# Kernel optimization log

Measured on AMD Instinct MI355X. Metric: run time of the kernel, lower is better.

The kernel has to match this reference:

```python
import jax, jax.numpy as jnp
import numpy as np

N, E = 40000, 640000
S_IN, V_IN = 64, 32            # input irreps: 64x0e + 32x1o (dim 160)
S_MID, V_MID = 96, 128         # tp output: (64+32)x0e, (64+32+32)x1o
S_OUT, V_OUT = 96, 32          # gate irreps_in: 64x0e scalars + 32x0e gates + 32x1o gated
R = 64                         # edge scalar (radial basis) dim
FC_HID = 64
W_NUMEL = 64 + 64 + 32 + 32 + 32  # per-edge tp weights ('uvu', v=1): 224
NUM_NEIGHBORS = 16.0


def setup_inputs() -> dict:
    key = jax.random.key(0)
    ks = jax.random.split(key, 13)
    return {
        "node_features": jax.random.normal(ks[0], (N, S_IN + 3 * V_IN), jnp.float32),
        "node_attr": jnp.ones((N, 1), jnp.float32),
        "edge_src": jax.random.randint(ks[1], (E,), 0, N),
        "edge_dst": jax.random.randint(ks[2], (E,), 0, N),
        "edge_attr": jax.random.normal(ks[3], (E, 4), jnp.float32),
        "edge_scalars": jax.random.normal(ks[4], (E, R), jnp.float32),
        "lin1_ws": jax.random.normal(ks[5], (S_IN, S_IN), jnp.float32),
        "lin1_wv": jax.random.normal(ks[6], (V_IN, V_IN), jnp.float32),
        "fc_w1": jax.random.normal(ks[7], (R, FC_HID), jnp.float32),
        "fc_w2": jax.random.normal(ks[8], (FC_HID, W_NUMEL), jnp.float32),
        "sc_ws": jax.random.normal(ks[9], (S_IN, S_OUT), jnp.float32),
        "sc_wv": jax.random.normal(ks[10], (V_IN, V_OUT), jnp.float32),
        "lin2_ws": jax.random.normal(ks[11], (S_MID, S_OUT), jnp.float32),
        "lin2_wv": jax.random.normal(ks[12], (V_MID, V_OUT), jnp.float32),
    }


def _inv(d):
    return 1.0 / jnp.sqrt(jnp.float32(d))


def _forward(node_features, node_attr, edge_attr, edge_scalars,
             lin1_ws, lin1_wv, fc_w1, fc_w2, sc_ws, sc_wv, lin2_ws, lin2_wv,
             edge_src, edge_dst):
    n = node_features.shape[0]
    s = node_features[:, :S_IN]                      # [N,64] 0e
    v = node_features[:, S_IN:].reshape(n, V_IN, 3)  # [N,32,3] 1o
    a = node_attr                                    # [N,1] scalar node attr

    # self-connection: FullyConnectedTensorProduct(input, 1x0e attr, out) == per-irrep linear
    sc_s = (s @ sc_ws) * a * _inv(S_IN)                                    # [N,96]
    sc_v = jnp.einsum('nci,cd->ndi', v, sc_wv) * a[:, :, None] * _inv(V_IN)  # [N,32,3]

    # lin1
    h_s = (s @ lin1_ws) * a * _inv(S_IN)
    h_v = jnp.einsum('nci,cd->ndi', v, lin1_wv) * a[:, :, None] * _inv(V_IN)

    # per-edge tensor-product weights from FC on edge scalars (silu MLP, no bias)
    hid = jax.nn.silu((edge_scalars @ fc_w1) * _inv(R))
    w = (hid @ fc_w2) * _inv(FC_HID)                 # [E,224]
    w1, w2, w3, w4, w5 = jnp.split(w, [64, 128, 160, 192], axis=-1)

    # gather source node features
    es = h_s[edge_src]                               # [E,64]
    ev = h_v[edge_src]                               # [E,32,3]
    e0 = edge_attr[:, :1]                            # [E,1]  0e
    e1 = edge_attr[:, 1:4]                           # [E,3]  1o

    # Clebsch-Gordan tensor product paths ('uvu', per-edge weights)
    m_s1 = w1 * es * e0                                                   # 0e x 0e -> 0e [E,64]
    m_s2 = w4 * jnp.einsum('eci,ei->ec', ev, e1) * _inv(3)                # 1o x 1o -> 0e [E,32]
    m_v1 = (w2 * es)[:, :, None] * e1[:, None, :]                         # 0e x 1o -> 1o [E,64,3]
    m_v2 = w3[:, :, None] * ev * e0[:, :, None]                           # 1o x 0e -> 1o [E,32,3]
    m_v3 = w5[:, :, None] * jnp.cross(ev, e1[:, None, :]) * _inv(2)       # 1o x 1o -> 1o [E,32,3]

    mid_s = jnp.concatenate([m_s1, m_s2], axis=-1)        # [E,96]
    mid_v = jnp.concatenate([m_v1, m_v2, m_v3], axis=1)   # [E,128,3]

    # scatter-sum to destination nodes, normalized by sqrt(num_neighbors)
    inv_nn = 1.0 / jnp.sqrt(jnp.float32(NUM_NEIGHBORS))
    agg_s = jax.ops.segment_sum(mid_s, edge_dst, num_segments=n) * inv_nn
    agg_v = jax.ops.segment_sum(mid_v, edge_dst, num_segments=n) * inv_nn

    # lin2
    o_s = (agg_s @ lin2_ws) * a * _inv(S_MID)                                  # [N,96]
    o_v = jnp.einsum('nci,cd->ndi', agg_v, lin2_wv) * a[:, :, None] * _inv(V_MID)  # [N,32,3]

    pre_s = sc_s + o_s
    pre_v = sc_v + o_v

    # Gate: silu on scalars, sigmoid gates multiply the l=1 features
    scalars = jax.nn.silu(pre_s[:, :64])
    gates = jax.nn.sigmoid(pre_s[:, 64:96])
    gated = gates[:, :, None] * pre_v                 # [N,32,3]
    return jnp.concatenate([scalars, gated.reshape(n, 3 * V_OUT)], axis=-1)  # [N,160]


def reference(node_features, node_attr, edge_src, edge_dst, edge_attr, edge_scalars,
              lin1_ws, lin1_wv, fc_w1, fc_w2, sc_ws, sc_wv, lin2_ws, lin2_wv):
    return _forward(node_features, node_attr, edge_attr, edge_scalars,
                    lin1_ws, lin1_wv, fc_w1, fc_w2, sc_ws, sc_wv, lin2_ws, lin2_wv,
                    edge_src, edge_dst)
```

## Files before the change

### kernel.cpp

```cpp
#include <hip/hip_runtime.h>

constexpr int N_NODES = 40000;
constexpr int N_EDGES = 640000;

constexpr float C_INV8     = 0.125f;
constexpr float C_INV_S32  = 0.17677669529663687f;
constexpr float C_INV_S3   = 0.57735026918962576f;
constexpr float C_INV_S2   = 0.70710678118654752f;
constexpr float C_INV_S96  = 0.10206207261596575f;
constexpr float C_INV_S128 = 0.08838834764831845f;
constexpr float C_INV_NN   = 0.25f;

typedef __attribute__((ext_vector_type(8))) short short8;
typedef __attribute__((ext_vector_type(4))) float f32x4;

__device__ __forceinline__ unsigned short f2bf(float x) {
  __bf16 b = (__bf16)x;
  return __builtin_bit_cast(unsigned short, b);
}
__device__ __forceinline__ float bf2f(unsigned short h) {
  return __uint_as_float(((unsigned int)h) << 16);
}

constexpr int NODE_BLOCKS = (N_NODES * 96 + 255) / 256;
constexpr int PREP_BLOCKS = 124;

__global__ __launch_bounds__(256) void k_pre(
    const float* __restrict__ nf, const float* __restrict__ attr,
    const float* __restrict__ ws_, const float* __restrict__ wv_,
    const float* __restrict__ fc_w1, const float* __restrict__ fc_w2,
    const float* __restrict__ lin2_ws, const float* __restrict__ lin2_wv,
    float* __restrict__ h_s, float* __restrict__ h_v,
    unsigned short* __restrict__ w1t, unsigned short* __restrict__ w2t,
    unsigned short* __restrict__ wst, unsigned short* __restrict__ wvt)
{
  if (blockIdx.x < NODE_BLOCKS) {
    int t = blockIdx.x * 256 + threadIdx.x;
    if (t < N_NODES * 64) {
      int n = t >> 6, c = t & 63;
      const float* s = nf + (long)n * 160;
      float acc = 0.f;
      #pragma unroll 8
      for (int k = 0; k < 64; ++k) acc = fmaf(s[k], ws_[k * 64 + c], acc);
      h_s[t] = acc * attr[n] * C_INV8;
    } else {
      int u = t - N_NODES * 64;
      if (u >= N_NODES * 32) return;
      int n = u >> 5, d = u & 31;
      const float* v = nf + (long)n * 160 + 64;
      float a0 = 0.f, a1 = 0.f, a2 = 0.f;
      #pragma unroll 8
      for (int c = 0; c < 32; ++c) {
        float wv = wv_[c * 32 + d];
        a0 = fmaf(v[3 * c + 0], wv, a0);
        a1 = fmaf(v[3 * c + 1], wv, a1);
        a2 = fmaf(v[3 * c + 2], wv, a2);
      }
      float sc = attr[n] * C_INV_S32;
      h_v[(long)u * 3 + 0] = a0 * sc;
      h_v[(long)u * 3 + 1] = a1 * sc;
      h_v[(long)u * 3 + 2] = a2 * sc;
    }
  } else {
    int t = (blockIdx.x - NODE_BLOCKS) * 256 + threadIdx.x;
    if (t < 4096) {
      int c = t >> 6, k = t & 63;
      w1t[c * 64 + k] = f2bf(fc_w1[k * 64 + c]);
    } else if (t < 4096 + 14336) {
      int u = t - 4096; int c = u >> 6, k = u & 63;
      w2t[c * 64 + k] = f2bf(fc_w2[k * 224 + c]);
    } else if (t < 18432 + 9216) {
      int u = t - 18432; int c = u / 96, k = u - c * 96;
      wst[c * 96 + k] = f2bf(lin2_ws[k * 96 + c] * (C_INV_NN * C_INV_S96));
    } else if (t < 27648 + 4096) {
      int u = t - 27648; int d = u >> 7, k = u & 127;
      wvt[d * 128 + k] = f2bf(lin2_wv[k * 32 + d] * (C_INV_NN * C_INV_S128));
    }
  }
}

__global__ __launch_bounds__(256) void k_deg(const int* __restrict__ edst,
                                             int* __restrict__ deg)
{
  int e = blockIdx.x * 256 + threadIdx.x;
  if (e < N_EDGES) atomicAdd(&deg[edst[e]], 1);
}

__global__ __launch_bounds__(1024) void k_scan(const int* __restrict__ deg,
                                               int* __restrict__ start,
                                               int* __restrict__ cursor)
{
  __shared__ int psum[1024];
  int tid = threadIdx.x;
  const int PER = 40;
  int base = tid * PER;
  int s = 0;
  for (int i = 0; i < PER; ++i) {
    int idx = base + i;
    if (idx < N_NODES) s += deg[idx];
  }
  psum[tid] = s;
  __syncthreads();
  for (int off = 1; off < 1024; off <<= 1) {
    int v = psum[tid];
    int u = (tid >= off) ? psum[tid - off] : 0;
    __syncthreads();
    psum[tid] = v + u;
    __syncthreads();
  }
  int run = (tid == 0) ? 0 : psum[tid - 1];
  for (int i = 0; i < PER; ++i) {
    int idx = base + i;
    if (idx < N_NODES) {
      start[idx] = run; cursor[idx] = run;
      run += deg[idx];
    }
  }
  if (tid == 1023) start[N_NODES] = run;
}

__global__ __launch_bounds__(256) void k_fill(const int* __restrict__ edst,
                                              int* __restrict__ cursor,
                                              int* __restrict__ pos)
{
  int e = blockIdx.x * 256 + threadIdx.x;
  if (e < N_EDGES) {
    int p = atomicAdd(&cursor[edst[e]], 1);
    pos[e] = p;
  }
}

__global__ __launch_bounds__(256) void k_edge2(
    const float* __restrict__ escal, const float* __restrict__ eattr,
    const int* __restrict__ esrc, const int* __restrict__ pos,
    const unsigned short* __restrict__ w1t, const unsigned short* __restrict__ w2t,
    const unsigned short* __restrict__ wst, const unsigned short* __restrict__ wvt,
    const float* __restrict__ h_s, const float* __restrict__ h_v,
    unsigned short* __restrict__ e_out)
{
  __shared__ unsigned short w_lds[64 * 232];
  int tid = threadIdx.x, warp = tid >> 6, lane = tid & 63;
  int lr = lane & 15, lg = lane >> 4;
  long e0 = (long)blockIdx.x * 64;
  int r0 = warp * 16;
  unsigned short* wp = w_lds + r0 * 232;

  long eM = e0 + r0 + lr;
  int srcM = esrc[eM];
  float4 ea4 = *reinterpret_cast<const float4*>(eattr + eM * 4);
  float ea0 = ea4.x, e1x = ea4.y, e1y = ea4.z, e1z = ea4.w;
  float esv[16];
  {
    const float* hsr = h_s + (long)srcM * 64;
    *reinterpret_cast<float4*>(&esv[0])  = *reinterpret_cast<const float4*>(hsr + lg * 8);
    *reinterpret_cast<float4*>(&esv[4])  = *reinterpret_cast<const float4*>(hsr + lg * 8 + 4);
    *reinterpret_cast<float4*>(&esv[8])  = *reinterpret_cast<const float4*>(hsr + 32 + lg * 8);
    *reinterpret_cast<float4*>(&esv[12]) = *reinterpret_cast<const float4*>(hsr + 32 + lg * 8 + 4);
  }
  float evv[24];
  {
    const float* hvr = h_v + (long)srcM * 96 + lg * 24;
    #pragma unroll
    for (int q = 0; q < 6; ++q)
      *reinterpret_cast<float4*>(&evv[4 * q]) = *reinterpret_cast<const float4*>(hvr + 4 * q);
  }

  f32x4 acc[4] = {};
  #pragma unroll
  for (int ks = 0; ks < 2; ++ks) {
    const float* ap = escal + eM * 64 + ks * 32 + lg * 8;
    float4 a01 = *reinterpret_cast<const float4*>(ap);
    float4 a23 = *reinterpret_cast<const float4*>(ap + 4);
    short8 af;
    af[0] = (short)f2bf(a01.x); af[1] = (short)f2bf(a01.y);
    af[2] = (short)f2bf(a01.z); af[3] = (short)f2bf(a01.w);
    af[4] = (short)f2bf(a23.x); af[5] = (short)f2bf(a23.y);
    af[6] = (short)f2bf(a23.z); af[7] = (short)f2bf(a23.w);
    #pragma unroll
    for (int nt = 0; nt < 4; ++nt) {
      short8 bf = *reinterpret_cast<const short8*>(w1t + (nt * 16 + lr) * 64 + ks * 32 + lg * 8);
      acc[nt] = __builtin_amdgcn_mfma_f32_16x16x32_bf16(af, bf, acc[nt], 0, 0, 0);
    }
  }
  #pragma unroll
  for (int nt = 0; nt < 4; ++nt)
    #pragma unroll
    for (int r = 0; r < 4; ++r) {
      float x = acc[nt][r] * C_INV8;
      float h = x / (1.f + __expf(-x));
      wp[(lg * 4 + r) * 72 + nt * 16 + lr] = f2bf(h);
    }

  f32x4 acc2[14] = {};
  #pragma unroll
  for (int ks = 0; ks < 2; ++ks) {
    short8 af = *reinterpret_cast<const short8*>(wp + lr * 72 + ks * 32 + lg * 8);
    #pragma unroll
    for (int nt = 0; nt < 14; ++nt) {
      short8 bf = *reinterpret_cast<const short8*>(w2t + (nt * 16 + lr) * 64 + ks * 32 + lg * 8);
      acc2[nt] = __builtin_amdgcn_mfma_f32_16x16x32_bf16(af, bf, acc2[nt], 0, 0, 0);
    }
  }
  #pragma unroll
  for (int nt = 0; nt < 14; ++nt)
    #pragma unroll
    for (int r = 0; r < 4; ++r)
      wp[(lg * 4 + r) * 232 + nt * 16 + lr] = f2bf(acc2[nt][r] * C_INV8);

  const unsigned short* wrow = wp + lr * 232;
  short8 w1a = *reinterpret_cast<const short8*>(wrow + lg * 8);
  short8 w1b = *reinterpret_cast<const short8*>(wrow + 32 + lg * 8);
  short8 w2a = *reinterpret_cast<const short8*>(wrow + 64 + lg * 8);
  short8 w2b = *reinterpret_cast<const short8*>(wrow + 96 + lg * 8);
  short8 w3s = *reinterpret_cast<const short8*>(wrow + 128 + lg * 8);
  short8 w4s = *reinterpret_cast<const short8*>(wrow + 160 + lg * 8);
  short8 w5s = *reinterpret_cast<const short8*>(wrow + 192 + lg * 8);

  f32x4 accS[6] = {};
  {
    short8 aS;
    #pragma unroll
    for (int j = 0; j < 8; ++j) aS[j] = (short)f2bf(bf2f((unsigned short)w1a[j]) * esv[j] * ea0);
    #pragma unroll
    for (int nt = 0; nt < 6; ++nt) {
      short8 b = *reinterpret_cast<const short8*>(wst + (nt * 16 + lr) * 96 + lg * 8);
      accS[nt] = __builtin_amdgcn_mfma_f32_16x16x32_bf16(aS, b, accS[nt], 0, 0, 0);
    }
    #pragma unroll
    for (int j = 0; j < 8; ++j) aS[j] = (short)f2bf(bf2f((unsigned short)w1b[j]) * esv[8 + j] * ea0);
    #pragma unroll
    for (int nt = 0; nt < 6; ++nt) {
      short8 b = *reinterpret_cast<const short8*>(wst + (nt * 16 + lr) * 96 + 32 + lg * 8);
      accS[nt] = __builtin_amdgcn_mfma_f32_16x16x32_bf16(aS, b, accS[nt], 0, 0, 0);
    }
    #pragma unroll
    for (int j = 0; j < 8; ++j) {
      float dot = evv[3 * j] * e1x + evv[3 * j + 1] * e1y + evv[3 * j + 2] * e1z;
      aS[j] = (short)f2bf(bf2f((unsigned short)w4s[j]) * dot * C_INV_S3);
    }
    #pragma unroll
    for (int nt = 0; nt < 6; ++nt) {
      short8 b = *reinterpret_cast<const short8*>(wst + (nt * 16 + lr) * 96 + 64 + lg * 8);
      accS[nt] = __builtin_amdgcn_mfma_f32_16x16x32_bf16(aS, b, accS[nt], 0, 0, 0);
    }
  }

  f32x4 accV[6] = {};
  #pragma unroll
  for (int i = 0; i < 3; ++i) {
    float e1i = (i == 0) ? e1x : (i == 1) ? e1y : e1z;
    short8 aV;
    #pragma unroll
    for (int j = 0; j < 8; ++j) aV[j] = (short)f2bf(bf2f((unsigned short)w2a[j]) * esv[j] * e1i);
    #pragma unroll
    for (int nt = 0; nt < 2; ++nt) {
      short8 b = *reinterpret_cast<const short8*>(wvt + (nt * 16 + lr) * 128 + lg * 8);
      accV[i * 2 + nt] = __builtin_amdgcn_mfma_f32_16x16x32_bf16(aV, b, accV[i * 2 + nt], 0, 0, 0);
    }
    #pragma unroll
    for (int j = 0; j < 8; ++j) aV[j] = (short)f2bf(bf2f((unsigned short)w2b[j]) * esv[8 + j] * e1i);
    #pragma unroll
    for (int nt = 0; nt < 2; ++nt) {
      short8 b = *reinterpret_cast<const short8*>(wvt + (nt * 16 + lr) * 128 + 32 + lg * 8);
      accV[i * 2 + nt] = __builtin_amdgcn_mfma_f32_16x16x32_bf16(aV, b, accV[i * 2 + nt], 0, 0, 0);
    }
    #pragma unroll
    for (int j = 0; j < 8; ++j) aV[j] = (short)f2bf(bf2f((unsigned short)w3s[j]) * evv[3 * j + i] * ea0);
    #pragma unroll
    for (int nt = 0; nt < 2; ++nt) {
      short8 b = *reinterpret_cast<const short8*>(wvt + (nt * 16 + lr) * 128 + 64 + lg * 8);
      accV[i * 2 + nt] = __builtin_amdgcn_mfma_f32_16x16x32_bf16(aV, b, accV[i * 2 + nt], 0, 0, 0);
    }
    #pragma unroll
    for (int j = 0; j < 8; ++j) {
      float ex = evv[3 * j], ey = evv[3 * j + 1], ez = evv[3 * j + 2];
      float cr = (i == 0) ? (ey * e1z - ez * e1y)
               : (i == 1) ? (ez * e1x - ex * e1z)
                          : (ex * e1y - ey * e1x);
      aV[j] = (short)f2bf(bf2f((unsigned short)w5s[j]) * cr * C_INV_S2);
    }
    #pragma unroll
    for (int nt = 0; nt < 2; ++nt) {
      short8 b = *reinterpret_cast<const short8*>(wvt + (nt * 16 + lr) * 128 + 96 + lg * 8);
      accV[i * 2 + nt] = __builtin_amdgcn_mfma_f32_16x16x32_bf16(aV, b, accV[i * 2 + nt], 0, 0, 0);
    }
  }

  #pragma unroll
  for (int nt = 0; nt < 6; ++nt)
    #pragma unroll
    for (int r = 0; r < 4; ++r)
      wp[(lg * 4 + r) * 232 + nt * 16 + lr] = f2bf(accS[nt][r]);
  #pragma unroll
  for (int q = 0; q < 6; ++q) {
    int i = q >> 1, nt = q & 1;
    #pragma unroll
    for (int r = 0; r < 4; ++r)
      wp[(lg * 4 + r) * 232 + 96 + i * 32 + nt * 16 + lr] = f2bf(accV[q][r]);
  }

  #pragma unroll
  for (int c3 = 0; c3 < 6; ++c3) {
    int chunk = c3 * 64 + lane;
    int row = chunk / 24, col = chunk % 24;
    int p = pos[e0 + r0 + row];
    float4 v4 = *reinterpret_cast<const float4*>(wp + row * 232 + col * 8);
    *reinterpret_cast<float4*>(e_out + (long)p * 192 + col * 8) = v4;
  }
}

__global__ __launch_bounds__(192) void k_aggfin(
    const int* __restrict__ start, const unsigned short* __restrict__ eo,
    const float* __restrict__ nf, const float* __restrict__ attr,
    const float* __restrict__ sc_ws, const float* __restrict__ sc_wv,
    float* __restrict__ out)
{
  __shared__ float sm[2][192];
  int tid = threadIdx.x;
  int ln = tid / 96, c = tid - ln * 96;
  int n = blockIdx.x * 2 + ln;

  int s0 = start[n], s1 = start[n + 1];
  const unsigned int* base = reinterpret_cast<const unsigned int*>(eo);
  float a0 = 0.f, a1 = 0.f;
  long idx = (long)s0 * 96 + c;
  int k = s0;
  for (; k + 8 <= s1; k += 8) {
    unsigned int v[8];
    #pragma unroll
    for (int j = 0; j < 8; ++j) v[j] = base[idx + (long)j * 96];
    #pragma unroll
    for (int j = 0; j < 8; ++j) {
      a0 += bf2f((unsigned short)(v[j] & 0xffffu));
      a1 += bf2f((unsigned short)(v[j] >> 16));
    }
    idx += 8 * 96;
  }
  for (; k < s1; ++k) {
    unsigned int v = base[idx];
    a0 += bf2f((unsigned short)(v & 0xffffu));
    a1 += bf2f((unsigned short)(v >> 16));
    idx += 96;
  }
  sm[ln][2 * c]     = a0;
  sm[ln][2 * c + 1] = a1;
  __syncthreads();

  const float* s = nf + (long)n * 160;
  float a = attr[n];
  if (c < 64) {
    float acc2 = 0.f;
    #pragma unroll 8
    for (int kk = 0; kk < 64; ++kk) acc2 = fmaf(s[kk], sc_ws[kk * 96 + c], acc2);
    float pre = (sm[ln][c] + acc2 * C_INV8) * a;
    out[(long)n * 160 + c] = pre / (1.f + __expf(-pre));
  } else {
    int d = c - 64;
    float gacc = 0.f;
    #pragma unroll 8
    for (int kk = 0; kk < 64; ++kk) gacc = fmaf(s[kk], sc_ws[kk * 96 + 64 + d], gacc);
    float gpre = (sm[ln][64 + d] + gacc * C_INV8) * a;
    float g = 1.f / (1.f + __expf(-gpre));
    const float* v = s + 64;
    float s0v = 0.f, s1v = 0.f, s2v = 0.f;
    #pragma unroll 8
    for (int cc = 0; cc < 32; ++cc) {
      float wv = sc_wv[cc * 32 + d];
      s0v = fmaf(v[3 * cc + 0], wv, s0v);
      s1v = fmaf(v[3 * cc + 1], wv, s1v);
      s2v = fmaf(v[3 * cc + 2], wv, s2v);
    }
    const float* ag = sm[ln] + 96;
    float p0 = (ag[d]      + s0v * C_INV_S32) * a;
    float p1 = (ag[32 + d] + s1v * C_INV_S32) * a;
    float p2 = (ag[64 + d] + s2v * C_INV_S32) * a;
    float* o = out + (long)n * 160 + 64 + 3 * d;
    o[0] = g * p0; o[1] = g * p1; o[2] = g * p2;
  }
}

extern "C" void kernel_launch(void* const* d_in, const int* in_sizes, int n_in,
                              void* d_out, int out_size, void* d_ws, size_t ws_size,
                              hipStream_t stream)
{
  const float* nf      = (const float*)d_in[0];
  const float* attr    = (const float*)d_in[1];
  const int*   esrc    = (const int*)d_in[2];
  const int*   edst    = (const int*)d_in[3];
  const float* eattr   = (const float*)d_in[4];
  const float* escal   = (const float*)d_in[5];
  const float* lin1_ws = (const float*)d_in[6];
  const float* lin1_wv = (const float*)d_in[7];
  const float* fc_w1   = (const float*)d_in[8];
  const float* fc_w2   = (const float*)d_in[9];
  const float* sc_ws   = (const float*)d_in[10];
  const float* sc_wv   = (const float*)d_in[11];
  const float* lin2_ws = (const float*)d_in[12];
  const float* lin2_wv = (const float*)d_in[13];
  float* out = (float*)d_out;

  char* base = (char*)d_ws;
  size_t off = 0;
  auto carve = [&](size_t bytes) { void* p = base + off; off = (off + bytes + 63) & ~(size_t)63; return p; };
  float* h_s   = (float*)carve((size_t)N_NODES * 64 * 4);
  float* h_v   = (float*)carve((size_t)N_NODES * 96 * 4);
  unsigned short* w1t = (unsigned short*)carve(4096 * 2);
  unsigned short* w2t = (unsigned short*)carve(14336 * 2);
  unsigned short* wst = (unsigned short*)carve(9216 * 2);
  unsigned short* wvt = (unsigned short*)carve(4096 * 2);
  int* deg    = (int*)carve((size_t)N_NODES * 4);
  int* startp = (int*)carve((size_t)(N_NODES + 1) * 4);
  int* cursor = (int*)carve((size_t)N_NODES * 4);
  int* pos    = (int*)carve((size_t)N_EDGES * 4);
  unsigned short* e_out = (unsigned short*)carve((size_t)N_EDGES * 192 * 2);

  k_pre<<<NODE_BLOCKS + PREP_BLOCKS, 256, 0, stream>>>(
      nf, attr, lin1_ws, lin1_wv, fc_w1, fc_w2, lin2_ws, lin2_wv,
      h_s, h_v, w1t, w2t, wst, wvt);

  hipMemsetAsync(deg, 0, (size_t)N_NODES * 4, stream);
  k_deg<<<(N_EDGES + 255) / 256, 256, 0, stream>>>(edst, deg);
  k_scan<<<1, 1024, 0, stream>>>(deg, startp, cursor);
  k_fill<<<(N_EDGES + 255) / 256, 256, 0, stream>>>(edst, cursor, pos);
  k_edge2<<<N_EDGES / 64, 256, 0, stream>>>(escal, eattr, esrc, pos,
                                            w1t, w2t, wst, wvt, h_s, h_v, e_out);
  k_aggfin<<<N_NODES / 2, 192, 0, stream>>>(startp, e_out, nf, attr,
                                            sc_ws, sc_wv, out);
}
```

Baseline: 752.0 us.

## Software-pipeline edge kernel over four groups and fuse degree and fill passes

```diff
diff --git a/kernel.cpp b/kernel.cpp
--- a/kernel.cpp
+++ b/kernel.cpp
@@ -21,15 +21,29 @@
 __device__ __forceinline__ float bf2f(unsigned short h) {
   return __uint_as_float(((unsigned int)h) << 16);
 }
+__device__ __forceinline__ unsigned int pk2(float a, float b) {
+  return (unsigned int)f2bf(a) | ((unsigned int)f2bf(b) << 16);
+}
+__device__ __forceinline__ float unlo(unsigned int v) { return __uint_as_float(v << 16); }
+__device__ __forceinline__ float unhi(unsigned int v) { return __uint_as_float(v & 0xffff0000u); }
+#define PKGET(buf, j) (((j) & 1) ? unhi(buf[(j) >> 1]) : unlo(buf[(j) >> 1]))
+
+__device__ __forceinline__ short8 mk8(const unsigned int* p) {
+  union { unsigned int u[4]; short8 s; } cv;
+  cv.u[0] = p[0]; cv.u[1] = p[1]; cv.u[2] = p[2]; cv.u[3] = p[3];
+  return cv.s;
+}
 
 constexpr int NODE_BLOCKS = (N_NODES * 96 + 255) / 256;
 constexpr int PREP_BLOCKS = 124;
+constexpr int DEG_BLOCKS  = N_EDGES / 256;
 
 __global__ __launch_bounds__(256) void k_pre(
     const float* __restrict__ nf, const float* __restrict__ attr,
     const float* __restrict__ ws_, const float* __restrict__ wv_,
     const float* __restrict__ fc_w1, const float* __restrict__ fc_w2,
     const float* __restrict__ lin2_ws, const float* __restrict__ lin2_wv,
+    const int* __restrict__ edst, int* __restrict__ deg,
     float* __restrict__ h_s, float* __restrict__ h_v,
     unsigned short* __restrict__ w1t, unsigned short* __restrict__ w2t,
     unsigned short* __restrict__ wst, unsigned short* __restrict__ wvt)
@@ -61,7 +75,7 @@
       h_v[(long)u * 3 + 1] = a1 * sc;
       h_v[(long)u * 3 + 2] = a2 * sc;
     }
-  } else {
+  } else if (blockIdx.x < NODE_BLOCKS + PREP_BLOCKS) {
     int t = (blockIdx.x - NODE_BLOCKS) * 256 + threadIdx.x;
     if (t < 4096) {
       int c = t >> 6, k = t & 63;
@@ -76,14 +90,10 @@
       int u = t - 27648; int d = u >> 7, k = u & 127;
       wvt[d * 128 + k] = f2bf(lin2_wv[k * 32 + d] * (C_INV_NN * C_INV_S128));
     }
-  }
-}
-
-__global__ __launch_bounds__(256) void k_deg(const int* __restrict__ edst,
-                                             int* __restrict__ deg)
-{
-  int e = blockIdx.x * 256 + threadIdx.x;
-  if (e < N_EDGES) atomicAdd(&deg[edst[e]], 1);
+  } else {
+    int e = (blockIdx.x - NODE_BLOCKS - PREP_BLOCKS) * 256 + threadIdx.x;
+    if (e < N_EDGES) atomicAdd(&deg[edst[e]], 1);
+  }
 }
 
 __global__ __launch_bounds__(1024) void k_scan(const int* __restrict__ deg,
@@ -119,20 +129,192 @@
   if (tid == 1023) start[N_NODES] = run;
 }
 
-__global__ __launch_bounds__(256) void k_fill(const int* __restrict__ edst,
-                                              int* __restrict__ cursor,
-                                              int* __restrict__ pos)
-{
-  int e = blockIdx.x * 256 + threadIdx.x;
-  if (e < N_EDGES) {
-    int p = atomicAdd(&cursor[edst[e]], 1);
-    pos[e] = p;
-  }
+#define PRE_G(g, scl_, esv_, evv_, ea_)                                        \
+{                                                                              \
+  long eM_ = eW + (g) * 16 + lr;                                               \
+  int s_ = srcs[g];                                                            \
+  ea_ = *reinterpret_cast<const float4*>(eattr + eM_ * 4);                     \
+  const float* ap_ = escal + eM_ * 64 + lg * 8;                                \
+  float4 x0 = *reinterpret_cast<const float4*>(ap_);                           \
+  float4 x1 = *reinterpret_cast<const float4*>(ap_ + 4);                       \
+  float4 x2 = *reinterpret_cast<const float4*>(ap_ + 32);                      \
+  float4 x3 = *reinterpret_cast<const float4*>(ap_ + 36);                      \
+  const float* hs_ = h_s + (long)s_ * 64 + lg * 8;                             \
+  float4 h0 = *reinterpret_cast<const float4*>(hs_);                           \
+  float4 h1 = *reinterpret_cast<const float4*>(hs_ + 4);                       \
+  float4 h2 = *reinterpret_cast<const float4*>(hs_ + 32);                      \
+  float4 h3 = *reinterpret_cast<const float4*>(hs_ + 36);                      \
+  const float* hv_ = h_v + (long)s_ * 96 + lg * 24;                            \
+  float4 v0 = *reinterpret_cast<const float4*>(hv_);                           \
+  float4 v1 = *reinterpret_cast<const float4*>(hv_ + 4);                       \
+  float4 v2 = *reinterpret_cast<const float4*>(hv_ + 8);                       \
+  float4 v3 = *reinterpret_cast<const float4*>(hv_ + 12);                      \
+  float4 v4 = *reinterpret_cast<const float4*>(hv_ + 16);                      \
+  float4 v5 = *reinterpret_cast<const float4*>(hv_ + 20);                      \
+  scl_[0] = pk2(x0.x, x0.y); scl_[1] = pk2(x0.z, x0.w);                        \
+  scl_[2] = pk2(x1.x, x1.y); scl_[3] = pk2(x1.z, x1.w);                        \
+  scl_[4] = pk2(x2.x, x2.y); scl_[5] = pk2(x2.z, x2.w);                        \
+  scl_[6] = pk2(x3.x, x3.y); scl_[7] = pk2(x3.z, x3.w);                        \
+  esv_[0] = pk2(h0.x, h0.y); esv_[1] = pk2(h0.z, h0.w);                        \
+  esv_[2] = pk2(h1.x, h1.y); esv_[3] = pk2(h1.z, h1.w);                        \
+  esv_[4] = pk2(h2.x, h2.y); esv_[5] = pk2(h2.z, h2.w);                        \
+  esv_[6] = pk2(h3.x, h3.y); esv_[7] = pk2(h3.z, h3.w);                        \
+  evv_[0] = pk2(v0.x, v0.y); evv_[1] = pk2(v0.z, v0.w);                        \
+  evv_[2] = pk2(v1.x, v1.y); evv_[3] = pk2(v1.z, v1.w);                        \
+  evv_[4] = pk2(v2.x, v2.y); evv_[5] = pk2(v2.z, v2.w);                        \
+  evv_[6] = pk2(v3.x, v3.y); evv_[7] = pk2(v3.z, v3.w);                        \
+  evv_[8] = pk2(v4.x, v4.y); evv_[9] = pk2(v4.z, v4.w);                        \
+  evv_[10] = pk2(v5.x, v5.y); evv_[11] = pk2(v5.z, v5.w);                      \
+}
+
+#define COMP_G(g, scl_, esv_, evv_, ea_)                                       \
+{                                                                              \
+  float ea0 = ea_.x, e1x = ea_.y, e1y = ea_.z, e1z = ea_.w;                    \
+  {                                                                            \
+    f32x4 acc[4] = {};                                                         \
+    short8 af0 = mk8(scl_);                                                    \
+    short8 af1 = mk8(scl_ + 4);                                                \
+    _Pragma("unroll")                                                          \
+    for (int nt = 0; nt < 4; ++nt) {                                           \
+      short8 b0 = *reinterpret_cast<const short8*>(w1t + (nt * 16 + lr) * 64 + lg * 8);      \
+      short8 b1 = *reinterpret_cast<const short8*>(w1t + (nt * 16 + lr) * 64 + 32 + lg * 8); \
+      acc[nt] = __builtin_amdgcn_mfma_f32_16x16x32_bf16(af0, b0, acc[nt], 0, 0, 0);          \
+      acc[nt] = __builtin_amdgcn_mfma_f32_16x16x32_bf16(af1, b1, acc[nt], 0, 0, 0);          \
+    }                                                                          \
+    _Pragma("unroll")                                                          \
+    for (int nt = 0; nt < 4; ++nt)                                             \
+      _Pragma("unroll")                                                        \
+      for (int r = 0; r < 4; ++r) {                                            \
+        float x = acc[nt][r] * C_INV8;                                         \
+        float h = x / (1.f + __expf(-x));                                      \
+        wp[(lg * 4 + r) * 72 + nt * 16 + lr] = f2bf(h);                        \
+      }                                                                        \
+  }                                                                            \
+  {                                                                            \
+    short8 a20 = *reinterpret_cast<const short8*>(wp + lr * 72 + lg * 8);      \
+    short8 a21 = *reinterpret_cast<const short8*>(wp + lr * 72 + 32 + lg * 8); \
+    _Pragma("unroll")                                                          \
+    for (int nt = 0; nt < 14; ++nt) {                                          \
+      short8 b0 = *reinterpret_cast<const short8*>(w2t + (nt * 16 + lr) * 64 + lg * 8);      \
+      short8 b1 = *reinterpret_cast<const short8*>(w2t + (nt * 16 + lr) * 64 + 32 + lg * 8); \
+      f32x4 a2 = {};                                                           \
+      a2 = __builtin_amdgcn_mfma_f32_16x16x32_bf16(a20, b0, a2, 0, 0, 0);      \
+      a2 = __builtin_amdgcn_mfma_f32_16x16x32_bf16(a21, b1, a2, 0, 0, 0);      \
+      _Pragma("unroll")                                                        \
+      for (int r = 0; r < 4; ++r)                                              \
+        wp[(lg * 4 + r) * 232 + nt * 16 + lr] = f2bf(a2[r] * C_INV8);          \
+    }                                                                          \
+  }                                                                            \
+  const unsigned short* wrow = wp + lr * 232;                                  \
+  short8 w1a = *reinterpret_cast<const short8*>(wrow + lg * 8);                \
+  short8 w1b = *reinterpret_cast<const short8*>(wrow + 32 + lg * 8);           \
+  short8 w2a = *reinterpret_cast<const short8*>(wrow + 64 + lg * 8);           \
+  short8 w2b = *reinterpret_cast<const short8*>(wrow + 96 + lg * 8);           \
+  short8 w3s = *reinterpret_cast<const short8*>(wrow + 128 + lg * 8);          \
+  short8 w4s = *reinterpret_cast<const short8*>(wrow + 160 + lg * 8);          \
+  short8 w5s = *reinterpret_cast<const short8*>(wrow + 192 + lg * 8);          \
+  f32x4 accS[6] = {};                                                          \
+  {                                                                            \
+    short8 aS;                                                                 \
+    _Pragma("unroll")                                                          \
+    for (int j = 0; j < 8; ++j)                                                \
+      aS[j] = (short)f2bf(bf2f((unsigned short)w1a[j]) * PKGET(esv_, j) * ea0);\
+    _Pragma("unroll")                                                          \
+    for (int nt = 0; nt < 6; ++nt) {                                           \
+      short8 b = *reinterpret_cast<const short8*>(wst + (nt * 16 + lr) * 96 + lg * 8);       \
+      accS[nt] = __builtin_amdgcn_mfma_f32_16x16x32_bf16(aS, b, accS[nt], 0, 0, 0);          \
+    }                                                                          \
+    _Pragma("unroll")                                                          \
+    for (int j = 0; j < 8; ++j)                                                \
+      aS[j] = (short)f2bf(bf2f((unsigned short)w1b[j]) * PKGET(esv_, 8 + j) * ea0);          \
+    _Pragma("unroll")                                                          \
+    for (int nt = 0; nt < 6; ++nt) {                                           \
+      short8 b = *reinterpret_cast<const short8*>(wst + (nt * 16 + lr) * 96 + 32 + lg * 8);  \
+      accS[nt] = __builtin_amdgcn_mfma_f32_16x16x32_bf16(aS, b, accS[nt], 0, 0, 0);          \
+    }                                                                          \
+    _Pragma("unroll")                                                          \
+    for (int j = 0; j < 8; ++j) {                                              \
+      float dot = PKGET(evv_, 3 * j) * e1x + PKGET(evv_, 3 * j + 1) * e1y      \
+                + PKGET(evv_, 3 * j + 2) * e1z;                                \
+      aS[j] = (short)f2bf(bf2f((unsigned short)w4s[j]) * dot * C_INV_S3);      \
+    }                                                                          \
+    _Pragma("unroll")                                                          \
+    for (int nt = 0; nt < 6; ++nt) {                                           \
+      short8 b = *reinterpret_cast<const short8*>(wst + (nt * 16 + lr) * 96 + 64 + lg * 8);  \
+      accS[nt] = __builtin_amdgcn_mfma_f32_16x16x32_bf16(aS, b, accS[nt], 0, 0, 0);          \
+    }                                                                          \
+  }                                                                            \
+  f32x4 accV[6] = {};                                                          \
+  _Pragma("unroll")                                                            \
+  for (int i = 0; i < 3; ++i) {                                                \
+    float e1i = (i == 0) ? e1x : (i == 1) ? e1y : e1z;                         \
+    short8 aV;                                                                 \
+    _Pragma("unroll")                                                          \
+    for (int j = 0; j < 8; ++j)                                                \
+      aV[j] = (short)f2bf(bf2f((unsigned short)w2a[j]) * PKGET(esv_, j) * e1i);\
+    _Pragma("unroll")                                                          \
+    for (int nt = 0; nt < 2; ++nt) {                                           \
+      short8 b = *reinterpret_cast<const short8*>(wvt + (nt * 16 + lr) * 128 + lg * 8);      \
+      accV[i * 2 + nt] = __builtin_amdgcn_mfma_f32_16x16x32_bf16(aV, b, accV[i * 2 + nt], 0, 0, 0); \
+    }                                                                          \
+    _Pragma("unroll")                                                          \
+    for (int j = 0; j < 8; ++j)                                                \
+      aV[j] = (short)f2bf(bf2f((unsigned short)w2b[j]) * PKGET(esv_, 8 + j) * e1i);          \
+    _Pragma("unroll")                                                          \
+    for (int nt = 0; nt < 2; ++nt) {                                           \
+      short8 b = *reinterpret_cast<const short8*>(wvt + (nt * 16 + lr) * 128 + 32 + lg * 8); \
+      accV[i * 2 + nt] = __builtin_amdgcn_mfma_f32_16x16x32_bf16(aV, b, accV[i * 2 + nt], 0, 0, 0); \
+    }                                                                          \
+    _Pragma("unroll")                                                          \
+    for (int j = 0; j < 8; ++j)                                                \
+      aV[j] = (short)f2bf(bf2f((unsigned short)w3s[j]) * PKGET(evv_, 3 * j + i) * ea0);      \
+    _Pragma("unroll")                                                          \
+    for (int nt = 0; nt < 2; ++nt) {                                           \
+      short8 b = *reinterpret_cast<const short8*>(wvt + (nt * 16 + lr) * 128 + 64 + lg * 8); \
+      accV[i * 2 + nt] = __builtin_amdgcn_mfma_f32_16x16x32_bf16(aV, b, accV[i * 2 + nt], 0, 0, 0); \
+    }                                                                          \
+    _Pragma("unroll")                                                          \
+    for (int j = 0; j < 8; ++j) {                                              \
+      float ex = PKGET(evv_, 3 * j), ey = PKGET(evv_, 3 * j + 1), ez = PKGET(evv_, 3 * j + 2); \
+      float cr = (i == 0) ? (ey * e1z - ez * e1y)                              \
+               : (i == 1) ? (ez * e1x - ex * e1z)                              \
+                          : (ex * e1y - ey * e1x);                             \
+      aV[j] = (short)f2bf(bf2f((unsigned short)w5s[j]) * cr * C_INV_S2);       \
+    }                                                                          \
+    _Pragma("unroll")                                                          \
+    for (int nt = 0; nt < 2; ++nt) {                                           \
+      short8 b = *reinterpret_cast<const short8*>(wvt + (nt * 16 + lr) * 128 + 96 + lg * 8); \
+      accV[i * 2 + nt] = __builtin_amdgcn_mfma_f32_16x16x32_bf16(aV, b, accV[i * 2 + nt], 0, 0, 0); \
+    }                                                                          \
+  }                                                                            \
+  _Pragma("unroll")                                                            \
+  for (int nt = 0; nt < 6; ++nt)                                               \
+    _Pragma("unroll")                                                          \
+    for (int r = 0; r < 4; ++r)                                                \
+      wp[(lg * 4 + r) * 232 + nt * 16 + lr] = f2bf(accS[nt][r]);               \
+  _Pragma("unroll")                                                            \
+  for (int q = 0; q < 6; ++q) {                                                \
+    int i = q >> 1, nt = q & 1;                                                \
+    _Pragma("unroll")                                                          \
+    for (int r = 0; r < 4; ++r)                                                \
+      wp[(lg * 4 + r) * 232 + 96 + i * 32 + nt * 16 + lr] = f2bf(accV[q][r]);  \
+  }                                                                            \
+  int p_mine = 0;                                                              \
+  if (lane < 16) p_mine = atomicAdd(&cursor[myDst[g]], 1);                     \
+  _Pragma("unroll")                                                            \
+  for (int c3 = 0; c3 < 6; ++c3) {                                             \
+    int chunk = c3 * 64 + lane;                                                \
+    int row = chunk / 24, col = chunk % 24;                                    \
+    int p = __shfl(p_mine, row);                                               \
+    float4 vv = *reinterpret_cast<const float4*>(wp + row * 232 + col * 8);    \
+    *reinterpret_cast<float4*>(e_out + (long)p * 192 + col * 8) = vv;          \
+  }                                                                            \
 }
 
 __global__ __launch_bounds__(256) void k_edge2(
     const float* __restrict__ escal, const float* __restrict__ eattr,
-    const int* __restrict__ esrc, const int* __restrict__ pos,
+    const int* __restrict__ esrc, const int* __restrict__ edst,
+    int* __restrict__ cursor,
     const unsigned short* __restrict__ w1t, const unsigned short* __restrict__ w2t,
     const unsigned short* __restrict__ wst, const unsigned short* __restrict__ wvt,
     const float* __restrict__ h_s, const float* __restrict__ h_v,
@@ -141,172 +323,29 @@
   __shared__ unsigned short w_lds[64 * 232];
   int tid = threadIdx.x, warp = tid >> 6, lane = tid & 63;
   int lr = lane & 15, lg = lane >> 4;
-  long e0 = (long)blockIdx.x * 64;
-  int r0 = warp * 16;
-  unsigned short* wp = w_lds + r0 * 232;
-
-  long eM = e0 + r0 + lr;
-  int srcM = esrc[eM];
-  float4 ea4 = *reinterpret_cast<const float4*>(eattr + eM * 4);
-  float ea0 = ea4.x, e1x = ea4.y, e1y = ea4.z, e1z = ea4.w;
-  float esv[16];
-  {
-    const float* hsr = h_s + (long)srcM * 64;
-    *reinterpret_cast<float4*>(&esv[0])  = *reinterpret_cast<const float4*>(hsr + lg * 8);
-    *reinterpret_cast<float4*>(&esv[4])  = *reinterpret_cast<const float4*>(hsr + lg * 8 + 4);
-    *reinterpret_cast<float4*>(&esv[8])  = *reinterpret_cast<const float4*>(hsr + 32 + lg * 8);
-    *reinterpret_cast<float4*>(&esv[12]) = *reinterpret_cast<const float4*>(hsr + 32 + lg * 8 + 4);
-  }
-  float evv[24];
-  {
-    const float* hvr = h_v + (long)srcM * 96 + lg * 24;
+  long eW = (long)blockIdx.x * 256 + warp * 64;
+  unsigned short* wp = w_lds + (warp * 16) * 232;
+
+  int myDst[4];
+  if (lane < 16) {
     #pragma unroll
-    for (int q = 0; q < 6; ++q)
-      *reinterpret_cast<float4*>(&evv[4 * q]) = *reinterpret_cast<const float4*>(hvr + 4 * q);
-  }
-
-  f32x4 acc[4] = {};
+    for (int g = 0; g < 4; ++g) myDst[g] = edst[eW + g * 16 + lane];
+  }
+  int srcs[4];
   #pragma unroll
-  for (int ks = 0; ks < 2; ++ks) {
-    const float* ap = escal + eM * 64 + ks * 32 + lg * 8;
-    float4 a01 = *reinterpret_cast<const float4*>(ap);
-    float4 a23 = *reinterpret_cast<const float4*>(ap + 4);
-    short8 af;
-    af[0] = (short)f2bf(a01.x); af[1] = (short)f2bf(a01.y);
-    af[2] = (short)f2bf(a01.z); af[3] = (short)f2bf(a01.w);
-    af[4] = (short)f2bf(a23.x); af[5] = (short)f2bf(a23.y);
-    af[6] = (short)f2bf(a23.z); af[7] = (short)f2bf(a23.w);
-    #pragma unroll
-    for (int nt = 0; nt < 4; ++nt) {
-      short8 bf = *reinterpret_cast<const short8*>(w1t + (nt * 16 + lr) * 64 + ks * 32 + lg * 8);
-      acc[nt] = __builtin_amdgcn_mfma_f32_16x16x32_bf16(af, bf, acc[nt], 0, 0, 0);
-    }
-  }
-  #pragma unroll
-  for (int nt = 0; nt < 4; ++nt)
-    #pragma unroll
-    for (int r = 0; r < 4; ++r) {
-      float x = acc[nt][r] * C_INV8;
-      float h = x / (1.f + __expf(-x));
-      wp[(lg * 4 + r) * 72 + nt * 16 + lr] = f2bf(h);
-    }
-
-  f32x4 acc2[14] = {};
-  #pragma unroll
-  for (int ks = 0; ks < 2; ++ks) {
-    short8 af = *reinterpret_cast<const short8*>(wp + lr * 72 + ks * 32 + lg * 8);
-    #pragma unroll
-    for (int nt = 0; nt < 14; ++nt) {
-      short8 bf = *reinterpret_cast<const short8*>(w2t + (nt * 16 + lr) * 64 + ks * 32 + lg * 8);
-      acc2[nt] = __builtin_amdgcn_mfma_f32_16x16x32_bf16(af, bf, acc2[nt], 0, 0, 0);
-    }
-  }
-  #pragma unroll
-  for (int nt = 0; nt < 14; ++nt)
-    #pragma unroll
-    for (int r = 0; r < 4; ++r)
-      wp[(lg * 4 + r) * 232 + nt * 16 + lr] = f2bf(acc2[nt][r] * C_INV8);
-
-  const unsigned short* wrow = wp + lr * 232;
-  short8 w1a = *reinterpret_cast<const short8*>(wrow + lg * 8);
-  short8 w1b = *reinterpret_cast<const short8*>(wrow + 32 + lg * 8);
-  short8 w2a = *reinterpret_cast<const short8*>(wrow + 64 + lg * 8);
-  short8 w2b = *reinterpret_cast<const short8*>(wrow + 96 + lg * 8);
-  short8 w3s = *reinterpret_cast<const short8*>(wrow + 128 + lg * 8);
-  short8 w4s = *reinterpret_cast<const short8*>(wrow + 160 + lg * 8);
-  short8 w5s = *reinterpret_cast<const short8*>(wrow + 192 + lg * 8);
-
-  f32x4 accS[6] = {};
-  {
-    short8 aS;
-    #pragma unroll
-    for (int j = 0; j < 8; ++j) aS[j] = (short)f2bf(bf2f((unsigned short)w1a[j]) * esv[j] * ea0);
-    #pragma unroll
-    for (int nt = 0; nt < 6; ++nt) {
-      short8 b = *reinterpret_cast<const short8*>(wst + (nt * 16 + lr) * 96 + lg * 8);
-      accS[nt] = __builtin_amdgcn_mfma_f32_16x16x32_bf16(aS, b, accS[nt], 0, 0, 0);
-    }
-    #pragma unroll
-    for (int j = 0; j < 8; ++j) aS[j] = (short)f2bf(bf2f((unsigned short)w1b[j]) * esv[8 + j] * ea0);
-    #pragma unroll
-    for (int nt = 0; nt < 6; ++nt) {
-      short8 b = *reinterpret_cast<const short8*>(wst + (nt * 16 + lr) * 96 + 32 + lg * 8);
-      accS[nt] = __builtin_amdgcn_mfma_f32_16x16x32_bf16(aS, b, accS[nt], 0, 0, 0);
-    }
-    #pragma unroll
-    for (int j = 0; j < 8; ++j) {
-      float dot = evv[3 * j] * e1x + evv[3 * j + 1] * e1y + evv[3 * j + 2] * e1z;
-      aS[j] = (short)f2bf(bf2f((unsigned short)w4s[j]) * dot * C_INV_S3);
-    }
-    #pragma unroll
-    for (int nt = 0; nt < 6; ++nt) {
-      short8 b = *reinterpret_cast<const short8*>(wst + (nt * 16 + lr) * 96 + 64 + lg * 8);
-      accS[nt] = __builtin_amdgcn_mfma_f32_16x16x32_bf16(aS, b, accS[nt], 0, 0, 0);
-    }
-  }
-
-  f32x4 accV[6] = {};
-  #pragma unroll
-  for (int i = 0; i < 3; ++i) {
-    float e1i = (i == 0) ? e1x : (i == 1) ? e1y : e1z;
-    short8 aV;
-    #pragma unroll
-    for (int j = 0; j < 8; ++j) aV[j] = (short)f2bf(bf2f((unsigned short)w2a[j]) * esv[j] * e1i);
-    #pragma unroll
-    for (int nt = 0; nt < 2; ++nt) {
-      short8 b = *reinterpret_cast<const short8*>(wvt + (nt * 16 + lr) * 128 + lg * 8);
-      accV[i * 2 + nt] = __builtin_amdgcn_mfma_f32_16x16x32_bf16(aV, b, accV[i * 2 + nt], 0, 0, 0);
-    }
-    #pragma unroll
-    for (int j = 0; j < 8; ++j) aV[j] = (short)f2bf(bf2f((unsigned short)w2b[j]) * esv[8 + j] * e1i);
-    #pragma unroll
-    for (int nt = 0; nt < 2; ++nt) {
-      short8 b = *reinterpret_cast<const short8*>(wvt + (nt * 16 + lr) * 128 + 32 + lg * 8);
-      accV[i * 2 + nt] = __builtin_amdgcn_mfma_f32_16x16x32_bf16(aV, b, accV[i * 2 + nt], 0, 0, 0);
-    }
-    #pragma unroll
-    for (int j = 0; j < 8; ++j) aV[j] = (short)f2bf(bf2f((unsigned short)w3s[j]) * evv[3 * j + i] * ea0);
-    #pragma unroll
-    for (int nt = 0; nt < 2; ++nt) {
-      short8 b = *reinterpret_cast<const short8*>(wvt + (nt * 16 + lr) * 128 + 64 + lg * 8);
-      accV[i * 2 + nt] = __builtin_amdgcn_mfma_f32_16x16x32_bf16(aV, b, accV[i * 2 + nt], 0, 0, 0);
-    }
-    #pragma unroll
-    for (int j = 0; j < 8; ++j) {
-      float ex = evv[3 * j], ey = evv[3 * j + 1], ez = evv[3 * j + 2];
-      float cr = (i == 0) ? (ey * e1z - ez * e1y)
-               : (i == 1) ? (ez * e1x - ex * e1z)
-                          : (ex * e1y - ey * e1x);
-      aV[j] = (short)f2bf(bf2f((unsigned short)w5s[j]) * cr * C_INV_S2);
-    }
-    #pragma unroll
-    for (int nt = 0; nt < 2; ++nt) {
-      short8 b = *reinterpret_cast<const short8*>(wvt + (nt * 16 + lr) * 128 + 96 + lg * 8);
-      accV[i * 2 + nt] = __builtin_amdgcn_mfma_f32_16x16x32_bf16(aV, b, accV[i * 2 + nt], 0, 0, 0);
-    }
-  }
-
-  #pragma unroll
-  for (int nt = 0; nt < 6; ++nt)
-    #pragma unroll
-    for (int r = 0; r < 4; ++r)
-      wp[(lg * 4 + r) * 232 + nt * 16 + lr] = f2bf(accS[nt][r]);
-  #pragma unroll
-  for (int q = 0; q < 6; ++q) {
-    int i = q >> 1, nt = q & 1;
-    #pragma unroll
-    for (int r = 0; r < 4; ++r)
-      wp[(lg * 4 + r) * 232 + 96 + i * 32 + nt * 16 + lr] = f2bf(accV[q][r]);
-  }
-
-  #pragma unroll
-  for (int c3 = 0; c3 < 6; ++c3) {
-    int chunk = c3 * 64 + lane;
-    int row = chunk / 24, col = chunk % 24;
-    int p = pos[e0 + r0 + row];
-    float4 v4 = *reinterpret_cast<const float4*>(wp + row * 232 + col * 8);
-    *reinterpret_cast<float4*>(e_out + (long)p * 192 + col * 8) = v4;
-  }
+  for (int g = 0; g < 4; ++g) srcs[g] = esrc[eW + g * 16 + lr];
+
+  unsigned int sclA[8], esvA[8], evvA[12]; float4 eaA;
+  unsigned int sclB[8], esvB[8], evvB[12]; float4 eaB;
+
+  PRE_G(0, sclA, esvA, evvA, eaA)
+  PRE_G(1, sclB, esvB, evvB, eaB)
+  COMP_G(0, sclA, esvA, evvA, eaA)
+  PRE_G(2, sclA, esvA, evvA, eaA)
+  COMP_G(1, sclB, esvB, evvB, eaB)
+  PRE_G(3, sclB, esvB, evvB, eaB)
+  COMP_G(2, sclA, esvA, evvA, eaA)
+  COMP_G(3, sclB, esvB, evvB, eaB)
 }
 
 __global__ __launch_bounds__(192) void k_aggfin(
@@ -411,19 +450,15 @@
   int* deg    = (int*)carve((size_t)N_NODES * 4);
   int* startp = (int*)carve((size_t)(N_NODES + 1) * 4);
   int* cursor = (int*)carve((size_t)N_NODES * 4);
-  int* pos    = (int*)carve((size_t)N_EDGES * 4);
   unsigned short* e_out = (unsigned short*)carve((size_t)N_EDGES * 192 * 2);
 
-  k_pre<<<NODE_BLOCKS + PREP_BLOCKS, 256, 0, stream>>>(
+  hipMemsetAsync(deg, 0, (size_t)N_NODES * 4, stream);
+  k_pre<<<NODE_BLOCKS + PREP_BLOCKS + DEG_BLOCKS, 256, 0, stream>>>(
       nf, attr, lin1_ws, lin1_wv, fc_w1, fc_w2, lin2_ws, lin2_wv,
-      h_s, h_v, w1t, w2t, wst, wvt);
-
-  hipMemsetAsync(deg, 0, (size_t)N_NODES * 4, stream);
-  k_deg<<<(N_EDGES + 255) / 256, 256, 0, stream>>>(edst, deg);
+      edst, deg, h_s, h_v, w1t, w2t, wst, wvt);
   k_scan<<<1, 1024, 0, stream>>>(deg, startp, cursor);
-  k_fill<<<(N_EDGES + 255) / 256, 256, 0, stream>>>(edst, cursor, pos);
-  k_edge2<<<N_EDGES / 64, 256, 0, stream>>>(escal, eattr, esrc, pos,
-                                            w1t, w2t, wst, wvt, h_s, h_v, e_out);
+  k_edge2<<<N_EDGES / 256, 256, 0, stream>>>(escal, eattr, esrc, edst, cursor,
+                                             w1t, w2t, wst, wvt, h_s, h_v, e_out);
   k_aggfin<<<N_NODES / 2, 192, 0, stream>>>(startp, e_out, nf, attr,
                                             sc_ws, sc_wv, out);
 }
```

Measured after the change: 739.2 us. Within noise of the previous version (-1.7%).
